# Kernel optimization log

Measured on AMD Instinct MI355X. Metric: run time of the kernel, lower is better.

## Reference

```python
import jax, jax.numpy as jnp
import numpy as np

CP = (96, 96, 96)      # control-point grid size (D, H, W)
NSTEPS = 7             # VecInt int_steps
N_TP = 4               # timepoints
# all ordered pairs i<j: tid 'ti_to_tj' -> ref=i, flo=j  (K = 6)
REF_IDX = np.array([0, 0, 0, 1, 1, 2])
FLO_IDX = np.array([1, 2, 3, 2, 3, 3])


def _make_grid(shape):
    axes = [jnp.arange(s, dtype=jnp.float32) for s in shape]
    return jnp.stack(jnp.meshgrid(*axes, indexing='ij'), axis=0)  # (3, D, H, W)

GRID = _make_grid(CP)


def trilinear_sample(vol, coords):
    """Sample channels-first volume at absolute voxel coordinates.

    vol:    (C, D, H, W) field values
    coords: (3, D, H, W) absolute (i, j, k) voxel coordinates
    returns (C, D, H, W); border (clamp) handling at edges.
    """
    D, H, W = vol.shape[1:]
    x, y, z = coords[0], coords[1], coords[2]
    x0f = jnp.floor(x); y0f = jnp.floor(y); z0f = jnp.floor(z)
    fx = x - x0f; fy = y - y0f; fz = z - z0f
    x0 = jnp.clip(x0f.astype(jnp.int32), 0, D - 1)
    x1 = jnp.clip(x0 + 1, 0, D - 1)
    y0 = jnp.clip(y0f.astype(jnp.int32), 0, H - 1)
    y1 = jnp.clip(y0 + 1, 0, H - 1)
    z0 = jnp.clip(z0f.astype(jnp.int32), 0, W - 1)
    z1 = jnp.clip(z0 + 1, 0, W - 1)

    c000 = vol[:, x0, y0, z0]; c001 = vol[:, x0, y0, z1]
    c010 = vol[:, x0, y1, z0]; c011 = vol[:, x0, y1, z1]
    c100 = vol[:, x1, y0, z0]; c101 = vol[:, x1, y0, z1]
    c110 = vol[:, x1, y1, z0]; c111 = vol[:, x1, y1, z1]

    c00 = c000 * (1 - fz) + c001 * fz
    c01 = c010 * (1 - fz) + c011 * fz
    c10 = c100 * (1 - fz) + c101 * fz
    c11 = c110 * (1 - fz) + c111 * fz
    c0 = c00 * (1 - fy) + c01 * fy
    c1 = c10 * (1 - fy) + c11 * fy
    return c0 * (1 - fx) + c1 * fx


def vecint(v):
    """Scaling-and-squaring integration of stationary velocity field v: (3,D,H,W)."""
    v = v * (1.0 / 2.0 ** NSTEPS)
    for _ in range(NSTEPS):
        v = v + trilinear_sample(v, GRID + v)
    return v


def compose_fields(f1, f2):
    """(grid + f1 + f2(grid + f1)) - grid, fields (3,D,H,W)."""
    return f1 + trilinear_sample(f2, GRID + f1)


def setup_inputs() -> dict:
    key = jax.random.key(0)
    k1, k2 = jax.random.split(key)
    T = jax.random.normal(k1, (N_TP, 3) + CP, dtype=jnp.float32)
    R = jax.random.normal(k2, CP + (3, len(REF_IDX)), dtype=jnp.float32)
    return {"T": T, "R": R}


def reference(T, R):
    # integrate +/- velocity for every timepoint once (same math as per-pair calls)
    F_pos = jax.vmap(vecint)(T)           # (N, 3, D, H, W) = integrate(T[t])
    F_neg = jax.vmap(vecint)(-T)          # (N, 3, D, H, W) = integrate(-T[t])
    ref = jnp.asarray(REF_IDX)
    flo = jnp.asarray(FLO_IDX)
    # R_hat[k] = compose(integrate(-T[ref_k]), integrate(T[flo_k]))  -> (K,3,D,H,W)
    R_hat = jax.vmap(compose_fields)(F_neg[ref], F_pos[flo])
    # original permutes R_hat to (D,H,W,3,K); equivalently permute R the other way
    residue = R_hat - jnp.transpose(R, (4, 3, 0, 1, 2))  # (K,3,D,H,W)
    # l1 cost: sum_k,x sqrt(sum_c residue^2)
    loss = jnp.sum(jnp.sqrt(jnp.sum(residue ** 2, axis=1)))
    return loss
```

## Files before the change

kernel.cpp:

```cpp
#include <hip/hip_runtime.h>
#include <hip/hip_fp16.h>

#define NV    884736
#define NB    3456
#define DIM   96
#define DIM2  9216


union H4 { uint2 u; __half2 h2[2]; };
union H8 { uint4 u; __half2 h2[4]; };

__device__ __forceinline__ __half2 lerp_h2(__half2 lo, __half2 hi, __half2 t) {
    return __hfma2(t, __hsub2(hi, lo), lo);
}

struct TriW { int i00, i01, i10, i11; __half2 wx, wy, wz; };

__device__ __forceinline__ TriW tri_prep(float x, float y, float z) {
    TriW t;
    float xf = floorf(x), yf = floorf(y), zf = floorf(z);
    float fx = x - xf, fy = y - yf, fz = z - zf;
    int x0 = (int)xf; x0 = x0 < 0 ? 0 : (x0 > DIM - 1 ? DIM - 1 : x0);
    int y0 = (int)yf; y0 = y0 < 0 ? 0 : (y0 > DIM - 1 ? DIM - 1 : y0);
    int z0 = (int)zf; z0 = z0 < 0 ? 0 : (z0 > DIM - 1 ? DIM - 1 : z0);
    int x1 = x0 + 1; if (x1 > DIM - 1) x1 = DIM - 1;
    int y1 = y0 + 1; if (y1 > DIM - 1) y1 = DIM - 1;
    t.wx = __float2half2_rn(fx);
    t.wy = __float2half2_rn(fy);
    t.wz = __float2half2_rn(z0 < DIM - 1 ? fz : 0.0f);
    int X0 = x0 * DIM2, X1 = x1 * DIM2;
    int Y0 = y0 * DIM,  Y1 = y1 * DIM;
    t.i00 = X0 + Y0 + z0;  t.i01 = X0 + Y1 + z0;
    t.i10 = X1 + Y0 + z0;  t.i11 = X1 + Y1 + z0;
    return t;
}

__device__ __forceinline__ void tri_gather(const uint2* __restrict__ f,
                                           const TriW& t, H8 c[4]) {
    c[0].u = *(const uint4*)(f + t.i00);
    c[1].u = *(const uint4*)(f + t.i01);
    c[2].u = *(const uint4*)(f + t.i10);
    c[3].u = *(const uint4*)(f + t.i11);
}

struct H2P { __half2 xy, z; };

__device__ __forceinline__ H2P tri_combine(const TriW& t, const H8 c[4]) {
    __half2 xy00 = lerp_h2(c[0].h2[0], c[0].h2[2], t.wz);
    __half2 z_00 = lerp_h2(c[0].h2[1], c[0].h2[3], t.wz);
    __half2 xy01 = lerp_h2(c[1].h2[0], c[1].h2[2], t.wz);
    __half2 z_01 = lerp_h2(c[1].h2[1], c[1].h2[3], t.wz);
    __half2 xy10 = lerp_h2(c[2].h2[0], c[2].h2[2], t.wz);
    __half2 z_10 = lerp_h2(c[2].h2[1], c[2].h2[3], t.wz);
    __half2 xy11 = lerp_h2(c[3].h2[0], c[3].h2[2], t.wz);
    __half2 z_11 = lerp_h2(c[3].h2[1], c[3].h2[3], t.wz);
    __half2 xy0 = lerp_h2(xy00, xy01, t.wy);
    __half2 z_0 = lerp_h2(z_00, z_01, t.wy);
    __half2 xy1 = lerp_h2(xy10, xy11, t.wy);
    __half2 z_1 = lerp_h2(z_10, z_11, t.wy);
    H2P r;
    r.xy = lerp_h2(xy0, xy1, t.wx);
    r.z  = lerp_h2(z_0, z_1, t.wx);
    return r;
}

__global__ __launch_bounds__(256) void init_kernel(const float* __restrict__ T,
                                                   uint2* __restrict__ bufA,
                                                   float* __restrict__ out) {
    int t = blockIdx.y;
    int l = blockIdx.x * 256 + threadIdx.x;
    if (t == 0 && l == 0) out[0] = 0.0f;
    const float inv = 1.0f / 128.0f;
    float vx = T[(size_t)(t * 3 + 0) * NV + l] * inv;
    float vy = T[(size_t)(t * 3 + 1) * NV + l] * inv;
    float vz = T[(size_t)(t * 3 + 2) * NV + l] * inv;
    H4 p; p.h2[0] = __floats2half2_rn( vx,  vy); p.h2[1] = __floats2half2_rn( vz, 0.0f);
    H4 n; n.h2[0] = __floats2half2_rn(-vx, -vy); n.h2[1] = __floats2half2_rn(-vz, 0.0f);
    bufA[(size_t)t * NV + l]       = p.u;
    bufA[(size_t)(t + 4) * NV + l] = n.u;
}

__global__ __launch_bounds__(256) void step_kernel(const uint2* __restrict__ src,
                                                   uint2* __restrict__ dst) {
    int g  = blockIdx.x;
    int f  = g & 7;
    int vb = g >> 3;
    const uint2* __restrict__ s = src + (size_t)f * NV;
    uint2*       __restrict__ d = dst + (size_t)f * NV;

    int l   = vb * 256 + threadIdx.x;
    int i   = l / DIM2;
    int rem = l % DIM2;
    int j   = rem / DIM;
    int k   = rem % DIM;

    H4 v; v.u = s[l];
    float2 vxy = __half22float2(v.h2[0]);
    float  vz  = __low2float(v.h2[1]);

    TriW t = tri_prep((float)i + vxy.x, (float)j + vxy.y, (float)k + vz);
    H8 c[4];
    tri_gather(s, t, c);
    H2P smp = tri_combine(t, c);

    H4 o;
    o.h2[0] = __hadd2(v.h2[0], smp.xy);
    o.h2[1] = __hadd2(v.h2[1], smp.z);
    d[l] = o.u;
}

__global__ __launch_bounds__(256) void loss_kernel(const uint2* __restrict__ fields,
                                                   const float* __restrict__ R,
                                                   float* __restrict__ out) {
    int l = blockIdx.x * 256 + threadIdx.x;
    int k = l % DIM;
    int j = (l / DIM) % DIM;
    int i = l / DIM2;
    float fi = (float)i, fj = (float)j, fk = (float)k;

    H4 f1c[3];
    #pragma unroll
    for (int r = 0; r < 3; r++)
        f1c[r].u = fields[(size_t)(4 + r) * NV + l];

    float rbuf[18];
    const float* Rl = R + (size_t)l * 18;
    #pragma unroll
    for (int q = 0; q < 18; q++) rbuf[q] = Rl[q];

    const int REFI[6] = {0, 0, 0, 1, 1, 2};
    const int FLOI[6] = {1, 2, 3, 2, 3, 3};

    float acc = 0.0f;
    #pragma unroll
    for (int p = 0; p < 6; p++) {
        H4 f1 = f1c[REFI[p]];
        float2 f1xy = __half22float2(f1.h2[0]);
        float  f1z  = __low2float(f1.h2[1]);
        const uint2* __restrict__ f2 = fields + (size_t)FLOI[p] * NV;
        TriW t = tri_prep(fi + f1xy.x, fj + f1xy.y, fk + f1z);
        H8 c[4];
        tri_gather(f2, t, c);
        H2P s = tri_combine(t, c);
        __half2 hxy = __hadd2(f1.h2[0], s.xy);
        __half2 hz  = __hadd2(f1.h2[1], s.z);
        float2 sxy = __half22float2(hxy);
        float  sz  = __low2float(hz);
        float rx = sxy.x - rbuf[0 * 6 + p];
        float ry = sxy.y - rbuf[1 * 6 + p];
        float rz = sz    - rbuf[2 * 6 + p];
        acc += sqrtf(rx * rx + ry * ry + rz * rz);
    }

    __shared__ float wsum[4];
    int lane = threadIdx.x & 63;
    int wid  = threadIdx.x >> 6;
    #pragma unroll
    for (int off = 32; off > 0; off >>= 1)
        acc += __shfl_down(acc, off, 64);
    if (lane == 0) wsum[wid] = acc;
    __syncthreads();
    if (threadIdx.x == 0) {
        float s = wsum[0] + wsum[1] + wsum[2] + wsum[3];
        atomicAdd(out, s);
    }
}

extern "C" void kernel_launch(void* const* d_in, const int* in_sizes, int n_in,
                              void* d_out, int out_size, void* d_ws, size_t ws_size,
                              hipStream_t stream) {
    const float* T = (const float*)d_in[0];
    const float* R = (const float*)d_in[1];
    float* out = (float*)d_out;

    uint2* bufA = (uint2*)d_ws;
    uint2* bufB = bufA + (size_t)8 * NV + 32;

    dim3 blk(256);
    init_kernel<<<dim3(NB, 4), blk, 0, stream>>>(T, bufA, out);

    uint2* src = bufA;
    uint2* dst = bufB;
    for (int s = 0; s < 7; s++) {
        step_kernel<<<NB * 8, blk, 0, stream>>>(src, dst);
        uint2* tmp = src; src = dst; dst = tmp;
    }
    loss_kernel<<<NB, blk, 0, stream>>>(src, R, out);
}
```

Before: 404.9 us.

## Stage 12^3 tiles with halo in LDS for scaling-and-squaring steps

Replaces the per-voxel global-gather step kernel with a tiled kernel that loads a 12^3 block plus a halo (sized per step, growing as displacements grow) into shared memory, then samples the trilinear corners from LDS. When a sample falls outside the staged tile it falls back to global gathers. This aims to cut scattered global/L2 traffic, at the cost of redundant halo loads, a block barrier, and only 4096 blocks per launch.

```diff
diff --git a/kernel.cpp b/kernel.cpp
--- a/kernel.cpp
+++ b/kernel.cpp
@@ -5,19 +5,24 @@
 #define NB    3456
 #define DIM   96
 #define DIM2  9216
+#define TS    12
 
 
 union H4 { uint2 u; __half2 h2[2]; };
-union H8 { uint4 u; __half2 h2[4]; };
+struct H8 { __half2 h2[4]; };
 
 __device__ __forceinline__ __half2 lerp_h2(__half2 lo, __half2 hi, __half2 t) {
     return __hfma2(t, __hsub2(hi, lo), lo);
 }
 
-struct TriW { int i00, i01, i10, i11; __half2 wx, wy, wz; };
-
-__device__ __forceinline__ TriW tri_prep(float x, float y, float z) {
-    TriW t;
+__device__ __forceinline__ int clampi(int v) {
+    return v < 0 ? 0 : (v > DIM - 1 ? DIM - 1 : v);
+}
+
+struct TriP { int x0, y0, z0, x1, y1; __half2 wx, wy, wz; };
+
+__device__ __forceinline__ TriP tri_prep(float x, float y, float z) {
+    TriP t;
     float xf = floorf(x), yf = floorf(y), zf = floorf(z);
     float fx = x - xf, fy = y - yf, fz = z - zf;
     int x0 = (int)xf; x0 = x0 < 0 ? 0 : (x0 > DIM - 1 ? DIM - 1 : x0);
@@ -25,27 +30,28 @@
     int z0 = (int)zf; z0 = z0 < 0 ? 0 : (z0 > DIM - 1 ? DIM - 1 : z0);
     int x1 = x0 + 1; if (x1 > DIM - 1) x1 = DIM - 1;
     int y1 = y0 + 1; if (y1 > DIM - 1) y1 = DIM - 1;
+    t.x0 = x0; t.y0 = y0; t.z0 = z0; t.x1 = x1; t.y1 = y1;
     t.wx = __float2half2_rn(fx);
     t.wy = __float2half2_rn(fy);
     t.wz = __float2half2_rn(z0 < DIM - 1 ? fz : 0.0f);
-    int X0 = x0 * DIM2, X1 = x1 * DIM2;
-    int Y0 = y0 * DIM,  Y1 = y1 * DIM;
-    t.i00 = X0 + Y0 + z0;  t.i01 = X0 + Y1 + z0;
-    t.i10 = X1 + Y0 + z0;  t.i11 = X1 + Y1 + z0;
     return t;
 }
 
-__device__ __forceinline__ void tri_gather(const uint2* __restrict__ f,
-                                           const TriW& t, H8 c[4]) {
-    c[0].u = *(const uint4*)(f + t.i00);
-    c[1].u = *(const uint4*)(f + t.i01);
-    c[2].u = *(const uint4*)(f + t.i10);
-    c[3].u = *(const uint4*)(f + t.i11);
+__device__ __forceinline__ void tri_gather_global(const uint2* __restrict__ f,
+                                                  const TriP& t, H8 c[4]) {
+    int i00 = t.x0 * DIM2 + t.y0 * DIM + t.z0;
+    int i01 = t.x0 * DIM2 + t.y1 * DIM + t.z0;
+    int i10 = t.x1 * DIM2 + t.y0 * DIM + t.z0;
+    int i11 = t.x1 * DIM2 + t.y1 * DIM + t.z0;
+    *(uint4*)&c[0] = *(const uint4*)(f + i00);
+    *(uint4*)&c[1] = *(const uint4*)(f + i01);
+    *(uint4*)&c[2] = *(const uint4*)(f + i10);
+    *(uint4*)&c[3] = *(const uint4*)(f + i11);
 }
 
 struct H2P { __half2 xy, z; };
 
-__device__ __forceinline__ H2P tri_combine(const TriW& t, const H8 c[4]) {
+__device__ __forceinline__ H2P tri_combine(const TriP& t, const H8 c[4]) {
     __half2 xy00 = lerp_h2(c[0].h2[0], c[0].h2[2], t.wz);
     __half2 z_00 = lerp_h2(c[0].h2[1], c[0].h2[3], t.wz);
     __half2 xy01 = lerp_h2(c[1].h2[0], c[1].h2[2], t.wz);
@@ -80,33 +86,90 @@
     bufA[(size_t)(t + 4) * NV + l] = n.u;
 }
 
-__global__ __launch_bounds__(256) void step_kernel(const uint2* __restrict__ src,
-                                                   uint2* __restrict__ dst) {
-    int g  = blockIdx.x;
-    int f  = g & 7;
-    int vb = g >> 3;
+template<int HLO, int HHI>
+__global__ __launch_bounds__(256) void step_tile_kernel(const uint2* __restrict__ src,
+                                                        uint2* __restrict__ dst) {
+    constexpr int Lxy = TS + HLO + HHI;
+    constexpr int Lz  = Lxy + 1;
+    constexpr int R   = Lxy * Lxy;
+    constexpr int SZ  = R * Lz;
+    constexpr int LPR = (Lz <= 16) ? 16 : 32;
+    constexpr int RPI = 256 / LPR;
+    constexpr int NIT = (R + RPI - 1) / RPI;
+    __shared__ uint2 tile[SZ];
+
+    int b = blockIdx.x;
+    int f = b & 7;
+    int t = b >> 3;
+    int tz = t & 7, ty = (t >> 3) & 7, tx = t >> 6;
+    int gx0 = tx * TS, gy0 = ty * TS, gz0 = tz * TS;
+    int ox = gx0 - HLO, oy = gy0 - HLO, oz = gz0 - HLO;
+
     const uint2* __restrict__ s = src + (size_t)f * NV;
     uint2*       __restrict__ d = dst + (size_t)f * NV;
 
-    int l   = vb * 256 + threadIdx.x;
-    int i   = l / DIM2;
-    int rem = l % DIM2;
-    int j   = rem / DIM;
-    int k   = rem % DIM;
-
-    H4 v; v.u = s[l];
-    float2 vxy = __half22float2(v.h2[0]);
-    float  vz  = __low2float(v.h2[1]);
-
-    TriW t = tri_prep((float)i + vxy.x, (float)j + vxy.y, (float)k + vz);
-    H8 c[4];
-    tri_gather(s, t, c);
-    H2P smp = tri_combine(t, c);
-
-    H4 o;
-    o.h2[0] = __hadd2(v.h2[0], smp.xy);
-    o.h2[1] = __hadd2(v.h2[1], smp.z);
-    d[l] = o.u;
+    int rr = threadIdx.x / LPR;
+    int wz = threadIdx.x % LPR;
+    int gz = clampi(oz + wz);
+    #pragma unroll
+    for (int it = 0; it < NIT; it++) {
+        int r = it * RPI + rr;
+        if (r < R && wz < Lz) {
+            int lx = r / Lxy;
+            int ly = r - lx * Lxy;
+            int gx = clampi(ox + lx);
+            int gy = clampi(oy + ly);
+            tile[r * Lz + wz] = s[gx * DIM2 + gy * DIM + gz];
+        }
+    }
+    __syncthreads();
+
+    #pragma unroll
+    for (int it = 0; it < (TS * TS * TS + 255) / 256; it++) {
+        int n = it * 256 + threadIdx.x;
+        if (n >= TS * TS * TS) break;
+        int lz = n % TS;
+        int t1 = n / TS;
+        int ly = t1 % TS;
+        int lx = t1 / TS;
+        int gi = gx0 + lx, gj = gy0 + ly, gk = gz0 + lz;
+
+        H4 v;
+        v.u = tile[((lx + HLO) * Lxy + (ly + HLO)) * Lz + (lz + HLO)];
+        float2 vxy = __half22float2(v.h2[0]);
+        float  vz  = __low2float(v.h2[1]);
+        TriP p = tri_prep((float)gi + vxy.x, (float)gj + vxy.y, (float)gk + vz);
+
+        int lx0 = p.x0 - ox, lx1 = p.x1 - ox;
+        int ly0 = p.y0 - oy, ly1 = p.y1 - oy;
+        int lz0 = p.z0 - oz;
+        bool inb = (lx0 >= 0) & (lx1 <= Lxy - 1) &
+                   (ly0 >= 0) & (ly1 <= Lxy - 1) &
+                   (lz0 >= 0) & (lz0 <= Lz - 2);
+
+        H8 c[4];
+        if (inb) {
+            int b00 = (lx0 * Lxy + ly0) * Lz + lz0;
+            int b01 = (lx0 * Lxy + ly1) * Lz + lz0;
+            int b10 = (lx1 * Lxy + ly0) * Lz + lz0;
+            int b11 = (lx1 * Lxy + ly1) * Lz + lz0;
+            uint2 a0 = tile[b00], a1 = tile[b00 + 1];
+            uint2 b0 = tile[b01], b1 = tile[b01 + 1];
+            uint2 c0 = tile[b10], c1 = tile[b10 + 1];
+            uint2 d0 = tile[b11], d1 = tile[b11 + 1];
+            *(uint4*)&c[0] = make_uint4(a0.x, a0.y, a1.x, a1.y);
+            *(uint4*)&c[1] = make_uint4(b0.x, b0.y, b1.x, b1.y);
+            *(uint4*)&c[2] = make_uint4(c0.x, c0.y, c1.x, c1.y);
+            *(uint4*)&c[3] = make_uint4(d0.x, d0.y, d1.x, d1.y);
+        } else {
+            tri_gather_global(s, p, c);
+        }
+        H2P smp = tri_combine(p, c);
+        H4 o;
+        o.h2[0] = __hadd2(v.h2[0], smp.xy);
+        o.h2[1] = __hadd2(v.h2[1], smp.z);
+        d[gi * DIM2 + gj * DIM + gk] = o.u;
+    }
 }
 
 __global__ __launch_bounds__(256) void loss_kernel(const uint2* __restrict__ fields,
@@ -138,9 +201,9 @@
         float2 f1xy = __half22float2(f1.h2[0]);
         float  f1z  = __low2float(f1.h2[1]);
         const uint2* __restrict__ f2 = fields + (size_t)FLOI[p] * NV;
-        TriW t = tri_prep(fi + f1xy.x, fj + f1xy.y, fk + f1z);
+        TriP t = tri_prep(fi + f1xy.x, fj + f1xy.y, fk + f1z);
         H8 c[4];
-        tri_gather(f2, t, c);
+        tri_gather_global(f2, t, c);
         H2P s = tri_combine(t, c);
         __half2 hxy = __hadd2(f1.h2[0], s.xy);
         __half2 hz  = __hadd2(f1.h2[1], s.z);
@@ -181,9 +244,15 @@
 
     uint2* src = bufA;
     uint2* dst = bufB;
-    for (int s = 0; s < 7; s++) {
-        step_kernel<<<NB * 8, blk, 0, stream>>>(src, dst);
+    const int grid_tiles = 8 * 8 * 8 * 8;
+    for (int s = 0; s < 5; s++) {
+        step_tile_kernel<1, 1><<<grid_tiles, blk, 0, stream>>>(src, dst);
         uint2* tmp = src; src = dst; dst = tmp;
     }
+    step_tile_kernel<2, 2><<<grid_tiles, blk, 0, stream>>>(src, dst);
+    { uint2* tmp = src; src = dst; dst = tmp; }
+    step_tile_kernel<3, 3><<<grid_tiles, blk, 0, stream>>>(src, dst);
+    { uint2* tmp = src; src = dst; dst = tmp; }
+
     loss_kernel<<<NB, blk, 0, stream>>>(src, R, out);
 }
```

Measured after the change: 401.8 us. About the same (-0.8%).

## Stage halo tiles in shared memory for early scaling-squaring steps

Applied to the files above, without the earlier changes.

Adds a tiled step kernel that loads a 16xCYx16 brick plus halo of the field into LDS and does the trilinear gathers from shared memory, falling back to global loads when a sample lands outside the halo. The first five steps use halo 1 and the sixth uses halo 2, since displacements grow as the field is squared; the last step keeps the plain global-gather kernel. This aims to cut redundant global and L2 gather traffic, at the cost of a cooperative tile load, a barrier, LDS footprint that limits occupancy, and divergent fallback paths.

```diff
diff --git a/kernel.cpp b/kernel.cpp
--- a/kernel.cpp
+++ b/kernel.cpp
@@ -8,16 +8,20 @@
 
 
 union H4 { uint2 u; __half2 h2[2]; };
-union H8 { uint4 u; __half2 h2[4]; };
+struct H8 { __half2 h2[4]; };
 
 __device__ __forceinline__ __half2 lerp_h2(__half2 lo, __half2 hi, __half2 t) {
     return __hfma2(t, __hsub2(hi, lo), lo);
 }
 
-struct TriW { int i00, i01, i10, i11; __half2 wx, wy, wz; };
-
-__device__ __forceinline__ TriW tri_prep(float x, float y, float z) {
-    TriW t;
+__device__ __forceinline__ int clampi(int v) {
+    return v < 0 ? 0 : (v > DIM - 1 ? DIM - 1 : v);
+}
+
+struct TriP { int x0, y0, z0, x1, y1; __half2 wx, wy, wz; };
+
+__device__ __forceinline__ TriP tri_prep(float x, float y, float z) {
+    TriP t;
     float xf = floorf(x), yf = floorf(y), zf = floorf(z);
     float fx = x - xf, fy = y - yf, fz = z - zf;
     int x0 = (int)xf; x0 = x0 < 0 ? 0 : (x0 > DIM - 1 ? DIM - 1 : x0);
@@ -25,27 +29,28 @@
     int z0 = (int)zf; z0 = z0 < 0 ? 0 : (z0 > DIM - 1 ? DIM - 1 : z0);
     int x1 = x0 + 1; if (x1 > DIM - 1) x1 = DIM - 1;
     int y1 = y0 + 1; if (y1 > DIM - 1) y1 = DIM - 1;
+    t.x0 = x0; t.y0 = y0; t.z0 = z0; t.x1 = x1; t.y1 = y1;
     t.wx = __float2half2_rn(fx);
     t.wy = __float2half2_rn(fy);
     t.wz = __float2half2_rn(z0 < DIM - 1 ? fz : 0.0f);
-    int X0 = x0 * DIM2, X1 = x1 * DIM2;
-    int Y0 = y0 * DIM,  Y1 = y1 * DIM;
-    t.i00 = X0 + Y0 + z0;  t.i01 = X0 + Y1 + z0;
-    t.i10 = X1 + Y0 + z0;  t.i11 = X1 + Y1 + z0;
     return t;
 }
 
-__device__ __forceinline__ void tri_gather(const uint2* __restrict__ f,
-                                           const TriW& t, H8 c[4]) {
-    c[0].u = *(const uint4*)(f + t.i00);
-    c[1].u = *(const uint4*)(f + t.i01);
-    c[2].u = *(const uint4*)(f + t.i10);
-    c[3].u = *(const uint4*)(f + t.i11);
+__device__ __forceinline__ void tri_gather_global(const uint2* __restrict__ f,
+                                                  const TriP& t, H8 c[4]) {
+    int i00 = t.x0 * DIM2 + t.y0 * DIM + t.z0;
+    int i01 = t.x0 * DIM2 + t.y1 * DIM + t.z0;
+    int i10 = t.x1 * DIM2 + t.y0 * DIM + t.z0;
+    int i11 = t.x1 * DIM2 + t.y1 * DIM + t.z0;
+    *(uint4*)&c[0] = *(const uint4*)(f + i00);
+    *(uint4*)&c[1] = *(const uint4*)(f + i01);
+    *(uint4*)&c[2] = *(const uint4*)(f + i10);
+    *(uint4*)&c[3] = *(const uint4*)(f + i11);
 }
 
 struct H2P { __half2 xy, z; };
 
-__device__ __forceinline__ H2P tri_combine(const TriW& t, const H8 c[4]) {
+__device__ __forceinline__ H2P tri_combine(const TriP& t, const H8 c[4]) {
     __half2 xy00 = lerp_h2(c[0].h2[0], c[0].h2[2], t.wz);
     __half2 z_00 = lerp_h2(c[0].h2[1], c[0].h2[3], t.wz);
     __half2 xy01 = lerp_h2(c[1].h2[0], c[1].h2[2], t.wz);
@@ -80,8 +85,87 @@
     bufA[(size_t)(t + 4) * NV + l] = n.u;
 }
 
-__global__ __launch_bounds__(256) void step_kernel(const uint2* __restrict__ src,
-                                                   uint2* __restrict__ dst) {
+template<int H, int CY>
+__global__ __launch_bounds__(256) void step_col_kernel(const uint2* __restrict__ src,
+                                                       uint2* __restrict__ dst) {
+    constexpr int LX = 16 + 2 * H;
+    constexpr int LY = CY + 2 * H;
+    constexpr int LZ = 16 + 2 * H + 1;
+    constexpr int SZ = LX * LY * LZ;
+    constexpr int NTY = DIM / CY;
+    __shared__ uint2 tile[SZ];
+
+    int b = blockIdx.x;
+    int f = b & 7;
+    int t = b >> 3;
+    int tz = t % 6;
+    int t2 = t / 6;
+    int ty = t2 % NTY;
+    int tx = t2 / NTY;
+    int gx0 = tx * 16, gy0 = ty * CY, gz0 = tz * 16;
+    int ox = gx0 - H, oy = gy0 - H, oz = gz0 - H;
+
+    const uint2* __restrict__ s = src + (size_t)f * NV;
+    uint2*       __restrict__ d = dst + (size_t)f * NV;
+
+    for (int n = threadIdx.x; n < SZ; n += 256) {
+        int lz = n % LZ;
+        int r  = n / LZ;
+        int ly = r % LY;
+        int lx = r / LY;
+        tile[n] = s[clampi(ox + lx) * DIM2 + clampi(oy + ly) * DIM + clampi(oz + lz)];
+    }
+    __syncthreads();
+
+    int lz = threadIdx.x & 15;
+    int lx = threadIdx.x >> 4;
+    int gi = gx0 + lx, gk = gz0 + lz;
+    float fi = (float)gi, fk = (float)gk;
+    int own  = ((lx + H) * LY + H) * LZ + (lz + H);
+    int sidx = gi * DIM2 + gy0 * DIM + gk;
+
+    for (int q = 0; q < CY; q++) {
+        H4 v; v.u = tile[own];
+        float2 vxy = __half22float2(v.h2[0]);
+        float  vz  = __low2float(v.h2[1]);
+        TriP p = tri_prep(fi + vxy.x, (float)(gy0 + q) + vxy.y, fk + vz);
+
+        int a0 = p.x0 - ox, a1 = p.x1 - ox;
+        int b0 = p.y0 - oy, b1 = p.y1 - oy;
+        int c0 = p.z0 - oz;
+        bool inb = (a0 >= 0) & (a1 <= LX - 1) &
+                   (b0 >= 0) & (b1 <= LY - 1) &
+                   (c0 >= 0) & (c0 <= LZ - 2);
+
+        H8 c[4];
+        if (inb) {
+            int i00 = (a0 * LY + b0) * LZ + c0;
+            int i01 = (a0 * LY + b1) * LZ + c0;
+            int i10 = (a1 * LY + b0) * LZ + c0;
+            int i11 = (a1 * LY + b1) * LZ + c0;
+            uint2 A0 = tile[i00], A1 = tile[i00 + 1];
+            uint2 B0 = tile[i01], B1 = tile[i01 + 1];
+            uint2 C0 = tile[i10], C1 = tile[i10 + 1];
+            uint2 D0 = tile[i11], D1 = tile[i11 + 1];
+            *(uint4*)&c[0] = make_uint4(A0.x, A0.y, A1.x, A1.y);
+            *(uint4*)&c[1] = make_uint4(B0.x, B0.y, B1.x, B1.y);
+            *(uint4*)&c[2] = make_uint4(C0.x, C0.y, C1.x, C1.y);
+            *(uint4*)&c[3] = make_uint4(D0.x, D0.y, D1.x, D1.y);
+        } else {
+            tri_gather_global(s, p, c);
+        }
+        H2P smp = tri_combine(p, c);
+        H4 o;
+        o.h2[0] = __hadd2(v.h2[0], smp.xy);
+        o.h2[1] = __hadd2(v.h2[1], smp.z);
+        d[sidx] = o.u;
+        own  += LZ;
+        sidx += DIM;
+    }
+}
+
+__global__ __launch_bounds__(256) void step_plain_kernel(const uint2* __restrict__ src,
+                                                         uint2* __restrict__ dst) {
     int g  = blockIdx.x;
     int f  = g & 7;
     int vb = g >> 3;
@@ -98,9 +182,9 @@
     float2 vxy = __half22float2(v.h2[0]);
     float  vz  = __low2float(v.h2[1]);
 
-    TriW t = tri_prep((float)i + vxy.x, (float)j + vxy.y, (float)k + vz);
+    TriP t = tri_prep((float)i + vxy.x, (float)j + vxy.y, (float)k + vz);
     H8 c[4];
-    tri_gather(s, t, c);
+    tri_gather_global(s, t, c);
     H2P smp = tri_combine(t, c);
 
     H4 o;
@@ -138,9 +222,9 @@
         float2 f1xy = __half22float2(f1.h2[0]);
         float  f1z  = __low2float(f1.h2[1]);
         const uint2* __restrict__ f2 = fields + (size_t)FLOI[p] * NV;
-        TriW t = tri_prep(fi + f1xy.x, fj + f1xy.y, fk + f1z);
+        TriP t = tri_prep(fi + f1xy.x, fj + f1xy.y, fk + f1z);
         H8 c[4];
-        tri_gather(f2, t, c);
+        tri_gather_global(f2, t, c);
         H2P s = tri_combine(t, c);
         __half2 hxy = __hadd2(f1.h2[0], s.xy);
         __half2 hz  = __hadd2(f1.h2[1], s.z);
@@ -181,9 +265,14 @@
 
     uint2* src = bufA;
     uint2* dst = bufB;
-    for (int s = 0; s < 7; s++) {
-        step_kernel<<<NB * 8, blk, 0, stream>>>(src, dst);
+    for (int s = 0; s < 5; s++) {
+        step_col_kernel<1, 12><<<6 * 8 * 6 * 8, blk, 0, stream>>>(src, dst);
         uint2* tmp = src; src = dst; dst = tmp;
     }
+    step_col_kernel<2, 8><<<6 * 12 * 6 * 8, blk, 0, stream>>>(src, dst);
+    { uint2* tmp = src; src = dst; dst = tmp; }
+    step_plain_kernel<<<NB * 8, blk, 0, stream>>>(src, dst);
+    { uint2* tmp = src; src = dst; dst = tmp; }
+
     loss_kernel<<<NB, blk, 0, stream>>>(src, R, out);
 }
```

Result: slower. 439.2 us (+8.5%).
